# Performance work log

Measured on AMD Instinct MI355X. Metric: run time of the kernel, lower is better.

Reference implementation:

```python
import jax, jax.numpy as jnp
import numpy as np

N_NODES = 30000
N_EDGES = 480000
NODE_DIM = 16
NUM_RADIAL = 8
NUM_ELEMENTS = 120
R_MAX = 5.0
NUM_BLOCKS = 2
N_PATHS = 5  # h0*sh0->0e, h0*sh1->1o, h0*sh2->2e, h1.sh1->0e, h2.sh2->0e


def _sh_basis(u):
    # real spherical harmonics up to l=2, component normalization, on unit vectors u [E,3]
    x, y, z = u[:, 0], u[:, 1], u[:, 2]
    s15 = jnp.sqrt(jnp.asarray(15.0, u.dtype))
    s5 = jnp.sqrt(jnp.asarray(5.0, u.dtype))
    sh1 = jnp.sqrt(jnp.asarray(3.0, u.dtype)) * u                      # [E,3]
    sh2 = jnp.stack([s15 * x * y, s15 * y * z,
                     0.5 * s5 * (3.0 * z * z - 1.0),
                     s15 * x * z, 0.5 * s15 * (x * x - y * y)], -1)    # [E,5]
    return sh1, sh2


def _energy(pos, emb, W_init, Wr, br, W_out, W_read, W1, b1, W2, b2, z, edge_index):
    N = pos.shape[0]
    row, col = edge_index[0], edge_index[1]
    edge_vec = pos[row] - pos[col]                                     # [E,3] gather
    r = jnp.sqrt(jnp.sum(edge_vec * edge_vec, -1) + 1e-12)             # [E]
    n = jnp.arange(1, NUM_RADIAL + 1, dtype=pos.dtype)
    # Bessel radial basis: sqrt(2/rc) * sin(n*pi*r/rc)/r
    radial = jnp.sqrt(2.0 / R_MAX) * jnp.sin(n[None, :] * jnp.pi * r[:, None] / R_MAX) / r[:, None]  # [E,R]
    u = edge_vec / r[:, None]
    sh1, sh2 = _sh_basis(u)

    # initial projection: embedding scalars -> 0e channels; l=1,l=2 start at zero
    h0 = emb[z] @ W_init                                               # [N,C]
    h1 = jnp.zeros((N, NODE_DIM, 3), pos.dtype)
    h2 = jnp.zeros((N, NODE_DIM, 5), pos.dtype)

    for b in range(NUM_BLOCKS):
        w = (radial @ Wr[b] + br[b]).reshape(-1, N_PATHS, NODE_DIM)    # [E,P,C] radial path weights
        h0c, h1c, h2c = h0[col], h1[col], h2[col]
        # scalar messages: h0*sh0 + <h1,sh1> + <h2,sh2>
        m0 = (w[:, 0] * h0c
              + w[:, 3] * jnp.einsum('ecm,em->ec', h1c, sh1)
              + w[:, 4] * jnp.einsum('ecm,em->ec', h2c, sh2))          # [E,C]
        m1 = (w[:, 1] * h0c)[:, :, None] * sh1[:, None, :]             # [E,C,3]
        m2 = (w[:, 2] * h0c)[:, :, None] * sh2[:, None, :]             # [E,C,5]
        a0 = jax.ops.segment_sum(m0, row, num_segments=N)
        a1 = jax.ops.segment_sum(m1, row, num_segments=N)
        a2 = jax.ops.segment_sum(m2, row, num_segments=N)
        h0 = h0 + a0 @ W_out[b, 0]
        h1 = h1 + jnp.einsum('ncm,cd->ndm', a1, W_out[b, 1])
        h2 = h2 + jnp.einsum('ncm,cd->ndm', a2, W_out[b, 2])

    inv = h0 @ W_read                                                  # readout 0e part
    site = jax.nn.silu(inv @ W1 + b1) @ W2 + b2                        # [N,1]
    return jnp.sum(site)


def setup_inputs() -> dict:
    key = jax.random.key(0)
    ks = jax.random.split(key, 12)
    C, R = NODE_DIM, NUM_RADIAL
    s = 1.0 / np.sqrt(C)
    return {
        'pos': jax.random.normal(ks[0], (N_NODES, 3), jnp.float32) * 3.0,
        'z': jax.random.randint(ks[1], (N_NODES,), 0, NUM_ELEMENTS),
        'edge_index': jax.random.randint(ks[2], (2, N_EDGES), 0, N_NODES),
        'emb': jax.random.normal(ks[3], (NUM_ELEMENTS, C), jnp.float32),
        'W_init': jax.random.normal(ks[4], (C, C), jnp.float32) * s,
        'Wr': jax.random.normal(ks[5], (NUM_BLOCKS, R, N_PATHS * C), jnp.float32) / np.sqrt(R),
        'br': jnp.zeros((NUM_BLOCKS, N_PATHS * C), jnp.float32),
        'W_out': jax.random.normal(ks[6], (NUM_BLOCKS, 3, C, C), jnp.float32) * s,
        'W_read': jax.random.normal(ks[7], (C, C), jnp.float32) * s,
        'W1': jax.random.normal(ks[8], (C, C), jnp.float32) * s,
        'b1': jnp.zeros((C,), jnp.float32),
        'W2': jax.random.normal(ks[9], (C, 1), jnp.float32) * s,
        'b2': jnp.zeros((1,), jnp.float32),
    }


def reference(pos, z, edge_index, emb, W_init, Wr, br, W_out, W_read, W1, b1, W2, b2):
    e_fn = lambda p: _energy(p, emb, W_init, Wr, br, W_out, W_read, W1, b1, W2, b2, z, edge_index)
    total, dE_dpos = jax.value_and_grad(e_fn)(pos)
    energy = jnp.reshape(total, (1, 1))
    forces = -dE_dpos
    return energy, forces
```

## Files before the change

### kernel.cpp

```cpp
#include <hip/hip_runtime.h>
#include <math.h>

#ifndef M_PI
#define M_PI 3.14159265358979323846
#endif

static inline int cdiv(int a, int b){ return (a + b - 1) / b; }

#define SQRT3f  1.7320508075688772f
#define SQRT5f  2.23606797749979f
#define SQRT15f 3.872983346207417f
#define KRADf   0.6324555320336759f
#define PI5f    0.6283185307179586f

__device__ __forceinline__ float grp16_sum(float v){
  v += __shfl_xor(v, 1, 64);
  v += __shfl_xor(v, 2, 64);
  v += __shfl_xor(v, 4, 64);
  v += __shfl_xor(v, 8, 64);
  return v;
}
__device__ __forceinline__ float xgrp_sum(float v){
  v += __shfl_xor(v, 16, 64);
  v += __shfl_xor(v, 32, 64);
  return v;
}

__device__ __forceinline__ void sh_from_u(float ux, float uy, float uz,
                                          float* sh1, float* sh2)
{
  sh1[0] = SQRT3f*ux; sh1[1] = SQRT3f*uy; sh1[2] = SQRT3f*uz;
  sh2[0] = SQRT15f*ux*uy;
  sh2[1] = SQRT15f*uy*uz;
  sh2[2] = 0.5f*SQRT5f*(3.f*uz*uz - 1.f);
  sh2[3] = SQRT15f*ux*uz;
  sh2[4] = 0.5f*SQRT15f*(ux*ux - uy*uy);
}

__device__ __forceinline__ void rad_from_sc(float s1, float c1, float inv_r, float* rad)
{
  float tc = 2.f * c1;
  float sprev = 0.f, s = s1;
  float Ki = KRADf * inv_r;
  #pragma unroll
  for (int k = 0; k < 8; k++) {
    rad[k] = Ki * s;
    float sn = tc*s - sprev; sprev = s; s = sn;
  }
}
__device__ __forceinline__ void rad_drad_from_sc(float s1, float c1, float inv_r,
                                                 float* rad, float* draddr)
{
  float tc = 2.f * c1;
  float sprev = 0.f, s = s1, cprev = 1.f, cc = c1;
  float Ki = KRADf * inv_r;
  const float KPI5 = KRADf * PI5f;
  #pragma unroll
  for (int k = 0; k < 8; k++) {
    rad[k] = Ki * s;
    draddr[k] = (KPI5 * (float)(k+1) * cc - rad[k]) * inv_r;
    float sn = tc*s - sprev; sprev = s; s = sn;
    float cn = tc*cc - cprev; cprev = cc; cc = cn;
  }
}

__global__ void k_hist(const int* __restrict__ ei, int E,
                       int* __restrict__ deg_row, int* __restrict__ deg_col)
{
  int e = blockIdx.x * blockDim.x + threadIdx.x;
  if (e >= E) return;
  atomicAdd(&deg_row[ei[e]], 1);
  atomicAdd(&deg_col[ei[E + e]], 1);
}

__global__ void k_alloc(const int* __restrict__ deg_row, const int* __restrict__ deg_col,
                        int* __restrict__ start_row, int* __restrict__ cur_row,
                        int* __restrict__ start_col, int* __restrict__ cur_col,
                        int* __restrict__ cursors, int N)
{
  int idx = blockIdx.x * blockDim.x + threadIdx.x;
  int lane = threadIdx.x & 63;
  #pragma unroll
  for (int which = 0; which < 2; which++) {
    const int* deg = which ? deg_col : deg_row;
    int* start = which ? start_col : start_row;
    int* cur   = which ? cur_col   : cur_row;
    int v = (idx < N) ? deg[idx] : 0;
    int incl = v;
    #pragma unroll
    for (int d = 1; d < 64; d <<= 1) {
      int y = __shfl_up(incl, d, 64);
      if (lane >= d) incl += y;
    }
    int wtot = __shfl(incl, 63, 64);
    int base = 0;
    if (lane == 63) base = atomicAdd(&cursors[which], wtot);
    base = __shfl(base, 63, 64);
    if (idx < N) { int st = base + incl - v; start[idx] = st; cur[idx] = st; }
  }
}

__global__ void k_scatter_geom(const float* __restrict__ pos, const int* __restrict__ ei, int E,
                               int* __restrict__ cur_row, int* __restrict__ cur_col,
                               float4* __restrict__ uR, float2* __restrict__ scR,
                               float4* __restrict__ uC, float2* __restrict__ scC,
                               int* __restrict__ colR, int* __restrict__ cposR,
                               int* __restrict__ rowC, int* __restrict__ rposC)
{
  int e = blockIdx.x * blockDim.x + threadIdx.x;
  if (e >= E) return;
  int row = ei[e], col = ei[E + e];
  int pr = atomicAdd(&cur_row[row], 1);
  int pc = atomicAdd(&cur_col[col], 1);
  colR[pr] = col; cposR[pr] = pc;
  rowC[pc] = row; rposC[pc] = pr;

  float px = pos[row*3+0] - pos[col*3+0];
  float py = pos[row*3+1] - pos[col*3+1];
  float pz = pos[row*3+2] - pos[col*3+2];
  float r2 = px*px + py*py + pz*pz + 1e-12f;
  float r = sqrtf(r2);
  float inv_r = 1.0f / r;
  float ux = px*inv_r, uy = py*inv_r, uz = pz*inv_r;
  float s1, c1;
  sincosf(r * PI5f, &s1, &c1);
  float4 u4 = make_float4(ux, uy, uz, inv_r);
  float2 sc = make_float2(s1, c1);
  uR[pr] = u4; scR[pr] = sc;
  uC[pc] = u4; scC[pc] = sc;
}

__global__ void k_node_init(const float* __restrict__ emb, const int* __restrict__ z,
                            const float* __restrict__ W_init, float* __restrict__ h0, int N)
{
  __shared__ float sW[256];
  if (threadIdx.x < 256) sW[threadIdx.x] = W_init[threadIdx.x];
  __syncthreads();
  int n = blockIdx.x * blockDim.x + threadIdx.x;
  if (n >= N) return;
  const float* e = emb + z[n]*16;
  float ev[16];
  #pragma unroll
  for (int k = 0; k < 16; k++) ev[k] = e[k];
  #pragma unroll
  for (int c = 0; c < 16; c++) {
    float s = 0.f;
    #pragma unroll
    for (int k = 0; k < 16; k++) s += ev[k] * sW[k*16+c];
    h0[n*16+c] = s;
  }
}

__global__ void k_fwd_b0(const float* __restrict__ Wr, const float* __restrict__ br,
                         const float* __restrict__ h0_in,
                         const float4* __restrict__ uR, const float2* __restrict__ scR,
                         const int* __restrict__ colR,
                         const int* __restrict__ start_row, const int* __restrict__ deg_row,
                         float* __restrict__ a0, float* __restrict__ a1, float* __restrict__ a2,
                         int N)
{
  int n = (blockIdx.x * blockDim.x + threadIdx.x) >> 6;
  int lane = threadIdx.x & 63;
  int g = lane >> 4, c = lane & 15;
  if (n >= N) return;
  float wr0[8], wr1[8], wr2[8];
  #pragma unroll
  for (int k = 0; k < 8; k++) {
    wr0[k] = Wr[k*80 + c];
    wr1[k] = Wr[k*80 + 16 + c];
    wr2[k] = Wr[k*80 + 32 + c];
  }
  float b0v = br[c], b1v = br[16 + c], b2v = br[32 + c];

  float acc0 = 0.f, acc1[3] = {0.f,0.f,0.f}, acc2[5] = {0.f,0.f,0.f,0.f,0.f};

  int i0 = start_row[n] + g, i1 = start_row[n] + deg_row[n];
  float4 Un = {0,0,0,0}; float2 SCn = {0,0};
  float h0n = 0.f;
  if (i0 < i1) {
    Un = uR[i0]; SCn = scR[i0];
    h0n = h0_in[colR[i0]*16 + c];
  }
  for (int i = i0; i < i1; i += 4) {
    float4 U = Un; float2 SC = SCn;
    float h0c = h0n;
    if (i+4 < i1) {
      Un = uR[i+4]; SCn = scR[i+4];
      h0n = h0_in[colR[i+4]*16 + c];
    }
    float rad[8];
    rad_from_sc(SC.x, SC.y, U.w, rad);
    float sh1[3], sh2[5];
    sh_from_u(U.x, U.y, U.z, sh1, sh2);
    float w0 = b0v, w1 = b1v, w2 = b2v;
    #pragma unroll
    for (int k = 0; k < 8; k++) {
      w0 += rad[k]*wr0[k]; w1 += rad[k]*wr1[k]; w2 += rad[k]*wr2[k];
    }
    acc0 += w0*h0c;
    float wh1 = w1*h0c, wh2 = w2*h0c;
    #pragma unroll
    for (int m = 0; m < 3; m++) acc1[m] += wh1*sh1[m];
    #pragma unroll
    for (int m = 0; m < 5; m++) acc2[m] += wh2*sh2[m];
  }
  acc0 = xgrp_sum(acc0);
  #pragma unroll
  for (int m = 0; m < 3; m++) acc1[m] = xgrp_sum(acc1[m]);
  #pragma unroll
  for (int m = 0; m < 5; m++) acc2[m] = xgrp_sum(acc2[m]);
  if (g == 0) {
    a0[n*16 + c] = acc0;
    #pragma unroll
    for (int m = 0; m < 3; m++) a1[n*48 + c*3 + m] = acc1[m];
    #pragma unroll
    for (int m = 0; m < 5; m++) a2[n*80 + c*5 + m] = acc2[m];
  }
}

__global__ void k_fwd_b1(const float* __restrict__ Wr, const float* __restrict__ br,
                         const float* __restrict__ h0_in, const float* __restrict__ h1_in,
                         const float* __restrict__ h2_in,
                         const float4* __restrict__ uR, const float2* __restrict__ scR,
                         const int* __restrict__ colR,
                         const int* __restrict__ start_row, const int* __restrict__ deg_row,
                         float* __restrict__ a0, int N)
{
  int n = (blockIdx.x * blockDim.x + threadIdx.x) >> 6;
  int lane = threadIdx.x & 63;
  int g = lane >> 4, c = lane & 15;
  if (n >= N) return;
  float wr0[8], wr3[8], wr4[8];
  #pragma unroll
  for (int k = 0; k < 8; k++) {
    wr0[k] = Wr[k*80 + c];
    wr3[k] = Wr[k*80 + 48 + c];
    wr4[k] = Wr[k*80 + 64 + c];
  }
  float b0v = br[c], b3v = br[48 + c], b4v = br[64 + c];

  float acc0 = 0.f;
  int i0 = start_row[n] + g, i1 = start_row[n] + deg_row[n];
  float4 Un = {0,0,0,0}; float2 SCn = {0,0};
  float h0n = 0.f, h1n[3] = {0,0,0}, h2n[5] = {0,0,0,0,0};
  if (i0 < i1) {
    int col = colR[i0];
    Un = uR[i0]; SCn = scR[i0];
    h0n = h0_in[col*16 + c];
    #pragma unroll
    for (int m = 0; m < 3; m++) h1n[m] = h1_in[col*48 + c*3 + m];
    #pragma unroll
    for (int m = 0; m < 5; m++) h2n[m] = h2_in[col*80 + c*5 + m];
  }
  for (int i = i0; i < i1; i += 4) {
    float4 U = Un; float2 SC = SCn;
    float h0c = h0n;
    float h1c[3], h2c[5];
    #pragma unroll
    for (int m = 0; m < 3; m++) h1c[m] = h1n[m];
    #pragma unroll
    for (int m = 0; m < 5; m++) h2c[m] = h2n[m];
    if (i+4 < i1) {
      int col = colR[i+4];
      Un = uR[i+4]; SCn = scR[i+4];
      h0n = h0_in[col*16 + c];
      #pragma unroll
      for (int m = 0; m < 3; m++) h1n[m] = h1_in[col*48 + c*3 + m];
      #pragma unroll
      for (int m = 0; m < 5; m++) h2n[m] = h2_in[col*80 + c*5 + m];
    }
    float rad[8];
    rad_from_sc(SC.x, SC.y, U.w, rad);
    float sh1[3], sh2[5];
    sh_from_u(U.x, U.y, U.z, sh1, sh2);
    float w0 = b0v, w3 = b3v, w4 = b4v;
    #pragma unroll
    for (int k = 0; k < 8; k++) {
      w0 += rad[k]*wr0[k]; w3 += rad[k]*wr3[k]; w4 += rad[k]*wr4[k];
    }
    float S1 = 0.f, S2 = 0.f;
    #pragma unroll
    for (int m = 0; m < 3; m++) S1 += h1c[m]*sh1[m];
    #pragma unroll
    for (int m = 0; m < 5; m++) S2 += h2c[m]*sh2[m];
    acc0 += w0*h0c + w3*S1 + w4*S2;
  }
  acc0 = xgrp_sum(acc0);
  if (g == 0) a0[n*16 + c] = acc0;
}

__global__ void k_node_update(const float* __restrict__ h0_in,
                              const float* __restrict__ a0, const float* __restrict__ a1,
                              const float* __restrict__ a2,
                              const float* __restrict__ U,
                              float* __restrict__ h0_out, float* __restrict__ h1_out,
                              float* __restrict__ h2_out, int N)
{
  int idx = blockIdx.x * blockDim.x + threadIdx.x;
  int n = idx >> 4, d = idx & 15;
  if (n >= N) return;
  const float* U0 = U;
  const float* U1 = U + 256;
  const float* U2 = U + 512;
  float s = h0_in[n*16 + d];
  #pragma unroll
  for (int c = 0; c < 16; c++) s += a0[n*16 + c] * U0[c*16 + d];
  h0_out[n*16 + d] = s;
  float v1[3] = {0.f, 0.f, 0.f};
  #pragma unroll
  for (int c = 0; c < 16; c++) {
    float u = U1[c*16 + d];
    #pragma unroll
    for (int m = 0; m < 3; m++) v1[m] += a1[n*48 + c*3 + m] * u;
  }
  #pragma unroll
  for (int m = 0; m < 3; m++) h1_out[n*48 + d*3 + m] = v1[m];
  float v2[5] = {0.f, 0.f, 0.f, 0.f, 0.f};
  #pragma unroll
  for (int c = 0; c < 16; c++) {
    float u = U2[c*16 + d];
    #pragma unroll
    for (int m = 0; m < 5; m++) v2[m] += a2[n*80 + c*5 + m] * u;
  }
  #pragma unroll
  for (int m = 0; m < 5; m++) h2_out[n*80 + d*5 + m] = v2[m];
}

__global__ void __launch_bounds__(256, 1)
k_readout_bwd(const float* __restrict__ h0s1, const float* __restrict__ a0in,
              const float* __restrict__ W_read,
              const float* __restrict__ W1, const float* __restrict__ b1,
              const float* __restrict__ W2, const float* __restrict__ b2,
              const float* __restrict__ U0b1,
              float* __restrict__ g0, float* __restrict__ ga0,
              float* __restrict__ partials, int N)
{
  __shared__ float sWr[256], sW1[256], sU[256], sb1[16], sW2[16], sb2;
  __shared__ float swave[4];
  {
    int t = threadIdx.x;
    if (t < 256) { sWr[t] = W_read[t]; sW1[t] = W1[t]; sU[t] = U0b1[t]; }
    if (t < 16)  { sb1[t] = b1[t]; sW2[t] = W2[t]; }
    if (t == 0)  sb2 = b2[0];
  }
  __syncthreads();
  int n = blockIdx.x * blockDim.x + threadIdx.x;
  float site = 0.f;
  if (n < N) {
    float h[16], av[16], inv[16], dt[16], g0v[16];
    #pragma unroll
    for (int d = 0; d < 16; d++) av[d] = a0in[n*16 + d];
    #pragma unroll
    for (int d = 0; d < 16; d++) {
      float s = h0s1[n*16 + d];
      #pragma unroll
      for (int cc = 0; cc < 16; cc++) s += av[cc] * sU[cc*16 + d];
      h[d] = s;
    }
    #pragma unroll
    for (int j = 0; j < 16; j++) {
      float s = 0.f;
      #pragma unroll
      for (int d = 0; d < 16; d++) s += h[d] * sWr[d*16 + j];
      inv[j] = s;
    }
    site = sb2;
    #pragma unroll
    for (int c = 0; c < 16; c++) {
      float t = sb1[c];
      #pragma unroll
      for (int j = 0; j < 16; j++) t += inv[j] * sW1[j*16 + c];
      float sg = 1.f / (1.f + expf(-t));
      float w2v = sW2[c];
      site += t * sg * w2v;
      dt[c] = w2v * sg * (1.f + t * (1.f - sg));
    }
    float dinv[16];
    #pragma unroll
    for (int j = 0; j < 16; j++) {
      float s = 0.f;
      #pragma unroll
      for (int c = 0; c < 16; c++) s += dt[c] * sW1[j*16 + c];
      dinv[j] = s;
    }
    #pragma unroll
    for (int d = 0; d < 16; d++) {
      float s = 0.f;
      #pragma unroll
      for (int j = 0; j < 16; j++) s += dinv[j] * sWr[d*16 + j];
      g0v[d] = s;
      g0[n*16 + d] = s;
    }
    #pragma unroll
    for (int c = 0; c < 16; c++) {
      float s = 0.f;
      #pragma unroll
      for (int d = 0; d < 16; d++) s += g0v[d] * sU[c*16 + d];
      ga0[n*16 + c] = s;
    }
  }
  #pragma unroll
  for (int off = 32; off; off >>= 1) site += __shfl_down(site, off, 64);
  int wave = threadIdx.x >> 6;
  if ((threadIdx.x & 63) == 0) swave[wave] = site;
  __syncthreads();
  if (threadIdx.x == 0)
    partials[blockIdx.x] = swave[0] + swave[1] + swave[2] + swave[3];
}

__global__ void k_energy(const float* __restrict__ partials, int nb,
                         float* __restrict__ energy)
{
  int t = threadIdx.x;
  float s = 0.f;
  for (int i = t; i < nb; i += 128) s += partials[i];
  #pragma unroll
  for (int off = 32; off; off >>= 1) s += __shfl_down(s, off, 64);
  __shared__ float sw[2];
  if ((t & 63) == 0) sw[t >> 6] = s;
  __syncthreads();
  if (t == 0) energy[0] = sw[0] + sw[1];
}

__global__ void k_ga(const float* __restrict__ g0, const float* __restrict__ g1,
                     const float* __restrict__ g2, const float* __restrict__ U,
                     float* __restrict__ ga0, float* __restrict__ ga1, float* __restrict__ ga2,
                     int N)
{
  int idx = blockIdx.x * blockDim.x + threadIdx.x;
  int n = idx >> 4, c = idx & 15;
  if (n >= N) return;
  const float* U0 = U;
  const float* U1 = U + 256;
  const float* U2 = U + 512;
  float s = 0.f;
  #pragma unroll
  for (int d = 0; d < 16; d++) s += g0[n*16 + d] * U0[c*16 + d];
  ga0[n*16 + c] = s;
  float v1[3] = {0.f, 0.f, 0.f};
  #pragma unroll
  for (int d = 0; d < 16; d++) {
    float u = U1[c*16 + d];
    #pragma unroll
    for (int m = 0; m < 3; m++) v1[m] += g1[n*48 + d*3 + m] * u;
  }
  #pragma unroll
  for (int m = 0; m < 3; m++) ga1[n*48 + c*3 + m] = v1[m];
  float v2[5] = {0.f, 0.f, 0.f, 0.f, 0.f};
  #pragma unroll
  for (int d = 0; d < 16; d++) {
    float u = U2[c*16 + d];
    #pragma unroll
    for (int m = 0; m < 5; m++) v2[m] += g2[n*80 + d*5 + m] * u;
  }
  #pragma unroll
  for (int m = 0; m < 5; m++) ga2[n*80 + c*5 + m] = v2[m];
}

__global__ void k_bwd_b1_col(const float* __restrict__ Wr, const float* __restrict__ br,
                             const float* __restrict__ h0_in, const float* __restrict__ h1_in,
                             const float* __restrict__ h2_in,
                             const float* __restrict__ ga0,
                             const float4* __restrict__ uC, const float2* __restrict__ scC,
                             const int* __restrict__ rowC,
                             const int* __restrict__ start_col, const int* __restrict__ deg_col,
                             float* __restrict__ g0, float* __restrict__ g1, float* __restrict__ g2,
                             float* __restrict__ dv_col, int N)
{
  int n = (blockIdx.x * blockDim.x + threadIdx.x) >> 6;
  int lane = threadIdx.x & 63;
  int g = lane >> 4, c = lane & 15;
  if (n >= N) return;
  float wr0[8], wr3[8], wr4[8];
  #pragma unroll
  for (int k = 0; k < 8; k++) {
    wr0[k] = Wr[k*80 + c];
    wr3[k] = Wr[k*80 + 48 + c];
    wr4[k] = Wr[k*80 + 64 + c];
  }
  float b0v = br[c], b3v = br[48 + c], b4v = br[64 + c];

  float h0c = h0_in[n*16 + c];
  float h1c[3], h2c[5];
  #pragma unroll
  for (int m = 0; m < 3; m++) h1c[m] = h1_in[n*48 + c*3 + m];
  #pragma unroll
  for (int m = 0; m < 5; m++) h2c[m] = h2_in[n*80 + c*5 + m];

  float accg0 = 0.f, accg1[3] = {0.f,0.f,0.f}, accg2[5] = {0.f,0.f,0.f,0.f,0.f};

  int i0 = start_col[n] + g, i1 = start_col[n] + deg_col[n];
  float4 Un = {0,0,0,0}; float2 SCn = {0,0};
  float dm0n = 0.f;
  if (i0 < i1) {
    Un = uC[i0]; SCn = scC[i0];
    dm0n = ga0[rowC[i0]*16 + c];
  }
  for (int i = i0; i < i1; i += 4) {
    float4 U = Un; float2 SC = SCn;
    float dm0 = dm0n;
    if (i+4 < i1) {
      Un = uC[i+4]; SCn = scC[i+4];
      dm0n = ga0[rowC[i+4]*16 + c];
    }
    float rad[8], draddr[8];
    rad_drad_from_sc(SC.x, SC.y, U.w, rad, draddr);
    float ux = U.x, uy = U.y, uz = U.z, inv_r = U.w;
    float sh1[3], sh2[5];
    sh_from_u(ux, uy, uz, sh1, sh2);

    float w0 = b0v, w3 = b3v, w4 = b4v;
    #pragma unroll
    for (int k = 0; k < 8; k++) {
      w0 += rad[k]*wr0[k]; w3 += rad[k]*wr3[k]; w4 += rad[k]*wr4[k];
    }

    float S1 = 0.f, S2 = 0.f;
    #pragma unroll
    for (int m = 0; m < 3; m++) S1 += h1c[m]*sh1[m];
    #pragma unroll
    for (int m = 0; m < 5; m++) S2 += h2c[m]*sh2[m];

    float dw0 = dm0 * h0c;
    float dw3 = dm0 * S1;
    float dw4 = dm0 * S2;
    float t3 = dm0 * w3, t4 = dm0 * w4;

    accg0 += dm0 * w0;
    #pragma unroll
    for (int m = 0; m < 3; m++) accg1[m] += t3 * sh1[m];
    #pragma unroll
    for (int m = 0; m < 5; m++) accg2[m] += t4 * sh2[m];

    float q1x = t3*h1c[0], q1y = t3*h1c[1], q1z = t3*h1c[2];
    float q0 = t4*h2c[0], q1 = t4*h2c[1], q2 = t4*h2c[2], q3 = t4*h2c[3], q4 = t4*h2c[4];
    float gr = 0.f;
    #pragma unroll
    for (int k = 0; k < 8; k++)
      gr += (dw0*wr0[k] + dw3*wr3[k] + dw4*wr4[k]) * draddr[k];
    float gux = SQRT3f*q1x + SQRT15f*(uy*q0 + uz*q3 + ux*q4);
    float guy = SQRT3f*q1y + SQRT15f*(ux*q0 + uz*q1 - uy*q4);
    float guz = SQRT3f*q1z + SQRT15f*uy*q1 + 3.f*SQRT5f*uz*q2 + SQRT15f*ux*q3;

    gr  = grp16_sum(gr);
    gux = grp16_sum(gux);
    guy = grp16_sum(guy);
    guz = grp16_sum(guz);

    if (c == 0) {
      float gdotu = gux*ux + guy*uy + guz*uz;
      dv_col[i*3+0] = gr*ux + (gux - gdotu*ux)*inv_r;
      dv_col[i*3+1] = gr*uy + (guy - gdotu*uy)*inv_r;
      dv_col[i*3+2] = gr*uz + (guz - gdotu*uz)*inv_r;
    }
  }
  accg0 = xgrp_sum(accg0);
  #pragma unroll
  for (int m = 0; m < 3; m++) accg1[m] = xgrp_sum(accg1[m]);
  #pragma unroll
  for (int m = 0; m < 5; m++) accg2[m] = xgrp_sum(accg2[m]);
  if (g == 0) {
    g0[n*16 + c] += accg0;
    #pragma unroll
    for (int m = 0; m < 3; m++) g1[n*48 + c*3 + m] = accg1[m];
    #pragma unroll
    for (int m = 0; m < 5; m++) g2[n*80 + c*5 + m] = accg2[m];
  }
}

__global__ void k_bwd_b0_row(const float* __restrict__ Wr, const float* __restrict__ br,
                             const float* __restrict__ h0_in,
                             const float* __restrict__ ga0, const float* __restrict__ ga1,
                             const float* __restrict__ ga2,
                             const float4* __restrict__ uR, const float2* __restrict__ scR,
                             const int* __restrict__ colR,
                             const int* __restrict__ start_row, const int* __restrict__ deg_row,
                             float* __restrict__ dv_row, int N)
{
  int n = (blockIdx.x * blockDim.x + threadIdx.x) >> 6;
  int lane = threadIdx.x & 63;
  int g = lane >> 4, c = lane & 15;
  if (n >= N) return;
  float wr0[8], wr1[8], wr2[8];
  #pragma unroll
  for (int k = 0; k < 8; k++) {
    wr0[k] = Wr[k*80 + c];
    wr1[k] = Wr[k*80 + 16 + c];
    wr2[k] = Wr[k*80 + 32 + c];
  }
  float b1v = br[16 + c], b2v = br[32 + c];

  float dm0 = ga0[n*16 + c];
  float dm1[3], dm2[5];
  #pragma unroll
  for (int m = 0; m < 3; m++) dm1[m] = ga1[n*48 + c*3 + m];
  #pragma unroll
  for (int m = 0; m < 5; m++) dm2[m] = ga2[n*80 + c*5 + m];

  int i0 = start_row[n] + g, i1 = start_row[n] + deg_row[n];
  float4 Un = {0,0,0,0}; float2 SCn = {0,0};
  float h0n = 0.f;
  if (i0 < i1) {
    Un = uR[i0]; SCn = scR[i0];
    h0n = h0_in[colR[i0]*16 + c];
  }
  for (int i = i0; i < i1; i += 4) {
    float4 U = Un; float2 SC = SCn;
    float h0c = h0n;
    if (i+4 < i1) {
      Un = uR[i+4]; SCn = scR[i+4];
      h0n = h0_in[colR[i+4]*16 + c];
    }
    float rad[8], draddr[8];
    rad_drad_from_sc(SC.x, SC.y, U.w, rad, draddr);
    float ux = U.x, uy = U.y, uz = U.z, inv_r = U.w;
    float sh1[3], sh2[5];
    sh_from_u(ux, uy, uz, sh1, sh2);

    float w1 = b1v, w2v = b2v;
    #pragma unroll
    for (int k = 0; k < 8; k++) { w1 += rad[k]*wr1[k]; w2v += rad[k]*wr2[k]; }

    float T1 = 0.f, T2 = 0.f;
    #pragma unroll
    for (int m = 0; m < 3; m++) T1 += dm1[m]*sh1[m];
    #pragma unroll
    for (int m = 0; m < 5; m++) T2 += dm2[m]*sh2[m];

    float dw0 = dm0 * h0c;
    float dw1 = h0c * T1;
    float dw2 = h0c * T2;

    float w1h = w1*h0c, w2h = w2v*h0c;
    float q1x = dm1[0]*w1h, q1y = dm1[1]*w1h, q1z = dm1[2]*w1h;
    float q0 = dm2[0]*w2h, q1 = dm2[1]*w2h, q2 = dm2[2]*w2h, q3 = dm2[3]*w2h, q4 = dm2[4]*w2h;

    float gr = 0.f;
    #pragma unroll
    for (int k = 0; k < 8; k++)
      gr += (dw0*wr0[k] + dw1*wr1[k] + dw2*wr2[k]) * draddr[k];
    float gux = SQRT3f*q1x + SQRT15f*(uy*q0 + uz*q3 + ux*q4);
    float guy = SQRT3f*q1y + SQRT15f*(ux*q0 + uz*q1 - uy*q4);
    float guz = SQRT3f*q1z + SQRT15f*uy*q1 + 3.f*SQRT5f*uz*q2 + SQRT15f*ux*q3;

    gr  = grp16_sum(gr);
    gux = grp16_sum(gux);
    guy = grp16_sum(guy);
    guz = grp16_sum(guz);

    if (c == 0) {
      float gdotu = gux*ux + guy*uy + guz*uz;
      dv_row[i*3+0] = gr*ux + (gux - gdotu*ux)*inv_r;
      dv_row[i*3+1] = gr*uy + (guy - gdotu*uy)*inv_r;
      dv_row[i*3+2] = gr*uz + (guz - gdotu*uz)*inv_r;
    }
  }
}

__global__ void k_force(const int* __restrict__ start_row, const int* __restrict__ deg_row,
                        const int* __restrict__ cposR,
                        const int* __restrict__ start_col, const int* __restrict__ deg_col,
                        const int* __restrict__ rposC,
                        const float* __restrict__ dv_col, const float* __restrict__ dv_row,
                        float* __restrict__ force, int N)
{
  int n = blockIdx.x * blockDim.x + threadIdx.x;
  if (n >= N) return;
  float fx = 0.f, fy = 0.f, fz = 0.f;
  int c0 = start_col[n], c1 = c0 + deg_col[n];
  for (int i = c0; i < c1; i++) {
    int rp = rposC[i];
    fx += dv_col[i*3+0] + dv_row[rp*3+0];
    fy += dv_col[i*3+1] + dv_row[rp*3+1];
    fz += dv_col[i*3+2] + dv_row[rp*3+2];
  }
  int r0 = start_row[n], r1 = r0 + deg_row[n];
  for (int i = r0; i < r1; i++) {
    int cp = cposR[i];
    fx -= dv_row[i*3+0] + dv_col[cp*3+0];
    fy -= dv_row[i*3+1] + dv_col[cp*3+1];
    fz -= dv_row[i*3+2] + dv_col[cp*3+2];
  }
  force[n*3+0] = fx; force[n*3+1] = fy; force[n*3+2] = fz;
}

extern "C" void kernel_launch(void* const* d_in, const int* in_sizes, int n_in,
                              void* d_out, int out_size, void* d_ws, size_t ws_size,
                              hipStream_t stream)
{
  const float* pos    = (const float*)d_in[0];
  const int*   z      = (const int*)  d_in[1];
  const int*   ei     = (const int*)  d_in[2];
  const float* emb    = (const float*)d_in[3];
  const float* W_init = (const float*)d_in[4];
  const float* Wr     = (const float*)d_in[5];
  const float* br     = (const float*)d_in[6];
  const float* W_out  = (const float*)d_in[7];
  const float* W_read = (const float*)d_in[8];
  const float* W1     = (const float*)d_in[9];
  const float* b1     = (const float*)d_in[10];
  const float* W2     = (const float*)d_in[11];
  const float* b2     = (const float*)d_in[12];

  const int N = in_sizes[0] / 3;
  const int E = in_sizes[2] / 2;

  const int BLK = 256;
  const int NPB = BLK / 64;
  const int NB_READOUT = cdiv(N, BLK);

  float* f = (float*)d_ws;
  float4* uR  = (float4*)f; f += (size_t)E*4;
  float4* uC  = (float4*)f; f += (size_t)E*4;
  float2* scR = (float2*)f; f += (size_t)E*2;
  float2* scC = (float2*)f; f += (size_t)E*2;
  float* h0_s0 = f; f += (size_t)N*16;
  float* h0_s1 = f; f += (size_t)N*16;
  float* h1_s1 = f; f += (size_t)N*48;
  float* h2_s1 = f; f += (size_t)N*80;
  float* a0    = f; f += (size_t)N*16;
  float* a1    = f; f += (size_t)N*48;
  float* a2    = f; f += (size_t)N*80;
  float* ga0b1 = f; f += (size_t)N*16;
  float* g0    = f; f += (size_t)N*16;
  float* g1    = f; f += (size_t)N*48;
  float* g2    = f; f += (size_t)N*80;
  float* dv_c  = f; f += (size_t)E*3;
  float* dv_r  = f; f += (size_t)E*3;
  float* partials = f; f += (size_t)NB_READOUT;
  int* ip = (int*)f;
  int* cursors   = ip; ip += 2;
  int* deg_row   = ip; ip += N;
  int* deg_col   = ip; ip += N;
  int* start_row = ip; ip += N;
  int* start_col = ip; ip += N;
  int* cur_row   = ip; ip += N;
  int* cur_col   = ip; ip += N;
  int* colR      = ip; ip += E;
  int* cposR     = ip; ip += E;
  int* rowC      = ip; ip += E;
  int* rposC     = ip; ip += E;

  float* out    = (float*)d_out;
  float* energy = out;
  float* force  = out + 1;

  (void)hipMemsetAsync(cursors, 0, (size_t)(2 + 2*N) * sizeof(int), stream);

  k_hist<<<cdiv(E, BLK), BLK, 0, stream>>>(ei, E, deg_row, deg_col);
  k_alloc<<<cdiv(N, BLK), BLK, 0, stream>>>(deg_row, deg_col, start_row, cur_row,
                                            start_col, cur_col, cursors, N);
  k_scatter_geom<<<cdiv(E, BLK), BLK, 0, stream>>>(pos, ei, E, cur_row, cur_col,
                                                   uR, scR, uC, scC,
                                                   colR, cposR, rowC, rposC);

  k_node_init<<<cdiv(N, BLK), BLK, 0, stream>>>(emb, z, W_init, h0_s0, N);

  k_fwd_b0<<<cdiv(N, NPB), BLK, 0, stream>>>(Wr, br, h0_s0, uR, scR, colR,
                                             start_row, deg_row, a0, a1, a2, N);
  k_node_update<<<cdiv(N*16, BLK), BLK, 0, stream>>>(h0_s0, a0, a1, a2,
                                                     W_out, h0_s1, h1_s1, h2_s1, N);

  k_fwd_b1<<<cdiv(N, NPB), BLK, 0, stream>>>(Wr + 640, br + 80,
                                             h0_s1, h1_s1, h2_s1, uR, scR, colR,
                                             start_row, deg_row, a0, N);

  k_readout_bwd<<<NB_READOUT, BLK, 0, stream>>>(h0_s1, a0, W_read, W1, b1, W2, b2,
                                                W_out + 768, g0, ga0b1, partials, N);
  k_energy<<<1, 128, 0, stream>>>(partials, NB_READOUT, energy);

  k_bwd_b1_col<<<cdiv(N, NPB), BLK, 0, stream>>>(Wr + 640, br + 80,
                                                 h0_s1, h1_s1, h2_s1, ga0b1,
                                                 uC, scC, rowC, start_col, deg_col,
                                                 g0, g1, g2, dv_c, N);

  k_ga<<<cdiv(N*16, BLK), BLK, 0, stream>>>(g0, g1, g2, W_out, a0, a1, a2, N);
  k_bwd_b0_row<<<cdiv(N, NPB), BLK, 0, stream>>>(Wr, br, h0_s0,
                                                 a0, a1, a2, uR, scR, colR,
                                                 start_row, deg_row, dv_r, N);

  k_force<<<cdiv(N, BLK), BLK, 0, stream>>>(start_row, deg_row, cposR,
                                            start_col, deg_col, rposC,
                                            dv_c, dv_r, force, N);
}
```

Before: 497.3 us.

## Use grid-stride persistent waves, 2-channel lanes for edges, and parallel force reduction

Edge kernels become grid-stride loops over nodes with a fixed grid, so the per-lane radial weights are loaded once and reused across many nodes. Three of them map 8 lanes to 2 channels each with float2 loads, letting 8 edges run per wave instead of 4. The backward kernels fold the radial derivative into two scalar accumulators instead of keeping 8-element rad/drad arrays. The force kernel splits each node's edges across 16 lanes and reduces with shuffles. The cost is more registers per lane and a longer per-edge dependency chain.

Result: slower. 899.1 us (+80.8%).

```diff
diff --git a/kernel.cpp b/kernel.cpp
--- a/kernel.cpp
+++ b/kernel.cpp
@@ -12,6 +12,7 @@
 #define SQRT15f 3.872983346207417f
 #define KRADf   0.6324555320336759f
 #define PI5f    0.6283185307179586f
+#define KPI5f   (KRADf * PI5f)
 
 __device__ __forceinline__ float grp16_sum(float v){
   v += __shfl_xor(v, 1, 64);
@@ -20,6 +21,18 @@
   v += __shfl_xor(v, 8, 64);
   return v;
 }
+__device__ __forceinline__ float grp8_sum(float v){
+  v += __shfl_xor(v, 1, 64);
+  v += __shfl_xor(v, 2, 64);
+  v += __shfl_xor(v, 4, 64);
+  return v;
+}
+__device__ __forceinline__ float xgrp8_sum(float v){
+  v += __shfl_xor(v, 8, 64);
+  v += __shfl_xor(v, 16, 64);
+  v += __shfl_xor(v, 32, 64);
+  return v;
+}
 __device__ __forceinline__ float xgrp_sum(float v){
   v += __shfl_xor(v, 16, 64);
   v += __shfl_xor(v, 32, 64);
@@ -48,21 +61,7 @@
     float sn = tc*s - sprev; sprev = s; s = sn;
   }
 }
-__device__ __forceinline__ void rad_drad_from_sc(float s1, float c1, float inv_r,
-                                                 float* rad, float* draddr)
-{
-  float tc = 2.f * c1;
-  float sprev = 0.f, s = s1, cprev = 1.f, cc = c1;
-  float Ki = KRADf * inv_r;
-  const float KPI5 = KRADf * PI5f;
-  #pragma unroll
-  for (int k = 0; k < 8; k++) {
-    rad[k] = Ki * s;
-    draddr[k] = (KPI5 * (float)(k+1) * cc - rad[k]) * inv_r;
-    float sn = tc*s - sprev; sprev = s; s = sn;
-    float cn = tc*cc - cprev; cprev = cc; cc = cn;
-  }
-}
+
 
 __global__ void k_hist(const int* __restrict__ ei, int E,
                        int* __restrict__ deg_row, int* __restrict__ deg_col)
@@ -159,10 +158,10 @@
                          float* __restrict__ a0, float* __restrict__ a1, float* __restrict__ a2,
                          int N)
 {
-  int n = (blockIdx.x * blockDim.x + threadIdx.x) >> 6;
+  int wid = (blockIdx.x * blockDim.x + threadIdx.x) >> 6;
+  int nw  = (gridDim.x * blockDim.x) >> 6;
   int lane = threadIdx.x & 63;
   int g = lane >> 4, c = lane & 15;
-  if (n >= N) return;
   float wr0[8], wr1[8], wr2[8];
   #pragma unroll
   for (int k = 0; k < 8; k++) {
@@ -172,49 +171,51 @@
   }
   float b0v = br[c], b1v = br[16 + c], b2v = br[32 + c];
 
-  float acc0 = 0.f, acc1[3] = {0.f,0.f,0.f}, acc2[5] = {0.f,0.f,0.f,0.f,0.f};
-
-  int i0 = start_row[n] + g, i1 = start_row[n] + deg_row[n];
-  float4 Un = {0,0,0,0}; float2 SCn = {0,0};
-  float h0n = 0.f;
-  if (i0 < i1) {
-    Un = uR[i0]; SCn = scR[i0];
-    h0n = h0_in[colR[i0]*16 + c];
-  }
-  for (int i = i0; i < i1; i += 4) {
-    float4 U = Un; float2 SC = SCn;
-    float h0c = h0n;
-    if (i+4 < i1) {
-      Un = uR[i+4]; SCn = scR[i+4];
-      h0n = h0_in[colR[i+4]*16 + c];
-    }
-    float rad[8];
-    rad_from_sc(SC.x, SC.y, U.w, rad);
-    float sh1[3], sh2[5];
-    sh_from_u(U.x, U.y, U.z, sh1, sh2);
-    float w0 = b0v, w1 = b1v, w2 = b2v;
-    #pragma unroll
-    for (int k = 0; k < 8; k++) {
-      w0 += rad[k]*wr0[k]; w1 += rad[k]*wr1[k]; w2 += rad[k]*wr2[k];
-    }
-    acc0 += w0*h0c;
-    float wh1 = w1*h0c, wh2 = w2*h0c;
-    #pragma unroll
-    for (int m = 0; m < 3; m++) acc1[m] += wh1*sh1[m];
-    #pragma unroll
-    for (int m = 0; m < 5; m++) acc2[m] += wh2*sh2[m];
-  }
-  acc0 = xgrp_sum(acc0);
-  #pragma unroll
-  for (int m = 0; m < 3; m++) acc1[m] = xgrp_sum(acc1[m]);
-  #pragma unroll
-  for (int m = 0; m < 5; m++) acc2[m] = xgrp_sum(acc2[m]);
-  if (g == 0) {
-    a0[n*16 + c] = acc0;
-    #pragma unroll
-    for (int m = 0; m < 3; m++) a1[n*48 + c*3 + m] = acc1[m];
-    #pragma unroll
-    for (int m = 0; m < 5; m++) a2[n*80 + c*5 + m] = acc2[m];
+  for (int n = wid; n < N; n += nw) {
+    float acc0 = 0.f, acc1[3] = {0.f,0.f,0.f}, acc2[5] = {0.f,0.f,0.f,0.f,0.f};
+
+    int i0 = start_row[n] + g, i1 = start_row[n] + deg_row[n];
+    float4 Un = {0,0,0,0}; float2 SCn = {0,0};
+    float h0n = 0.f;
+    if (i0 < i1) {
+      Un = uR[i0]; SCn = scR[i0];
+      h0n = h0_in[colR[i0]*16 + c];
+    }
+    for (int i = i0; i < i1; i += 4) {
+      float4 U = Un; float2 SC = SCn;
+      float h0c = h0n;
+      if (i+4 < i1) {
+        Un = uR[i+4]; SCn = scR[i+4];
+        h0n = h0_in[colR[i+4]*16 + c];
+      }
+      float rad[8];
+      rad_from_sc(SC.x, SC.y, U.w, rad);
+      float sh1[3], sh2[5];
+      sh_from_u(U.x, U.y, U.z, sh1, sh2);
+      float w0 = b0v, w1 = b1v, w2 = b2v;
+      #pragma unroll
+      for (int k = 0; k < 8; k++) {
+        w0 += rad[k]*wr0[k]; w1 += rad[k]*wr1[k]; w2 += rad[k]*wr2[k];
+      }
+      acc0 += w0*h0c;
+      float wh1 = w1*h0c, wh2 = w2*h0c;
+      #pragma unroll
+      for (int m = 0; m < 3; m++) acc1[m] += wh1*sh1[m];
+      #pragma unroll
+      for (int m = 0; m < 5; m++) acc2[m] += wh2*sh2[m];
+    }
+    acc0 = xgrp_sum(acc0);
+    #pragma unroll
+    for (int m = 0; m < 3; m++) acc1[m] = xgrp_sum(acc1[m]);
+    #pragma unroll
+    for (int m = 0; m < 5; m++) acc2[m] = xgrp_sum(acc2[m]);
+    if (g == 0) {
+      a0[n*16 + c] = acc0;
+      #pragma unroll
+      for (int m = 0; m < 3; m++) a1[n*48 + c*3 + m] = acc1[m];
+      #pragma unroll
+      for (int m = 0; m < 5; m++) a2[n*80 + c*5 + m] = acc2[m];
+    }
   }
 }
 
@@ -226,67 +227,77 @@
                          const int* __restrict__ start_row, const int* __restrict__ deg_row,
                          float* __restrict__ a0, int N)
 {
-  int n = (blockIdx.x * blockDim.x + threadIdx.x) >> 6;
+  int wid = (blockIdx.x * blockDim.x + threadIdx.x) >> 6;
+  int nw  = (gridDim.x * blockDim.x) >> 6;
   int lane = threadIdx.x & 63;
-  int g = lane >> 4, c = lane & 15;
-  if (n >= N) return;
-  float wr0[8], wr3[8], wr4[8];
+  int g = lane >> 3, cl = lane & 7;
+  const float2* Wr2 = (const float2*)Wr;
+  const float2* br2 = (const float2*)br;
+  const float2* h0_2 = (const float2*)h0_in;
+  const float2* h1_2 = (const float2*)h1_in;
+  const float2* h2_2 = (const float2*)h2_in;
+
+  float2 wr0[8], wr3[8], wr4[8];
   #pragma unroll
   for (int k = 0; k < 8; k++) {
-    wr0[k] = Wr[k*80 + c];
-    wr3[k] = Wr[k*80 + 48 + c];
-    wr4[k] = Wr[k*80 + 64 + c];
-  }
-  float b0v = br[c], b3v = br[48 + c], b4v = br[64 + c];
-
-  float acc0 = 0.f;
-  int i0 = start_row[n] + g, i1 = start_row[n] + deg_row[n];
-  float4 Un = {0,0,0,0}; float2 SCn = {0,0};
-  float h0n = 0.f, h1n[3] = {0,0,0}, h2n[5] = {0,0,0,0,0};
-  if (i0 < i1) {
-    int col = colR[i0];
-    Un = uR[i0]; SCn = scR[i0];
-    h0n = h0_in[col*16 + c];
-    #pragma unroll
-    for (int m = 0; m < 3; m++) h1n[m] = h1_in[col*48 + c*3 + m];
-    #pragma unroll
-    for (int m = 0; m < 5; m++) h2n[m] = h2_in[col*80 + c*5 + m];
-  }
-  for (int i = i0; i < i1; i += 4) {
-    float4 U = Un; float2 SC = SCn;
-    float h0c = h0n;
-    float h1c[3], h2c[5];
-    #pragma unroll
-    for (int m = 0; m < 3; m++) h1c[m] = h1n[m];
-    #pragma unroll
-    for (int m = 0; m < 5; m++) h2c[m] = h2n[m];
-    if (i+4 < i1) {
-      int col = colR[i+4];
-      Un = uR[i+4]; SCn = scR[i+4];
-      h0n = h0_in[col*16 + c];
-      #pragma unroll
-      for (int m = 0; m < 3; m++) h1n[m] = h1_in[col*48 + c*3 + m];
-      #pragma unroll
-      for (int m = 0; m < 5; m++) h2n[m] = h2_in[col*80 + c*5 + m];
-    }
-    float rad[8];
-    rad_from_sc(SC.x, SC.y, U.w, rad);
-    float sh1[3], sh2[5];
-    sh_from_u(U.x, U.y, U.z, sh1, sh2);
-    float w0 = b0v, w3 = b3v, w4 = b4v;
-    #pragma unroll
-    for (int k = 0; k < 8; k++) {
-      w0 += rad[k]*wr0[k]; w3 += rad[k]*wr3[k]; w4 += rad[k]*wr4[k];
-    }
-    float S1 = 0.f, S2 = 0.f;
-    #pragma unroll
-    for (int m = 0; m < 3; m++) S1 += h1c[m]*sh1[m];
-    #pragma unroll
-    for (int m = 0; m < 5; m++) S2 += h2c[m]*sh2[m];
-    acc0 += w0*h0c + w3*S1 + w4*S2;
-  }
-  acc0 = xgrp_sum(acc0);
-  if (g == 0) a0[n*16 + c] = acc0;
+    wr0[k] = Wr2[k*40 + cl];
+    wr3[k] = Wr2[k*40 + 24 + cl];
+    wr4[k] = Wr2[k*40 + 32 + cl];
+  }
+  float2 b0v = br2[cl], b3v = br2[24 + cl], b4v = br2[32 + cl];
+
+  for (int n = wid; n < N; n += nw) {
+    float acc0x = 0.f, acc0y = 0.f;
+    int i0 = start_row[n] + g, i1 = start_row[n] + deg_row[n];
+    float4 Un = {0,0,0,0}; float2 SCn = {0,0};
+    float2 h0n = {0.f,0.f}; int coln = 0;
+    if (i0 < i1) {
+      coln = colR[i0];
+      Un = uR[i0]; SCn = scR[i0];
+      h0n = h0_2[coln*8 + cl];
+    }
+    for (int i = i0; i < i1; i += 8) {
+      float4 U = Un; float2 SC = SCn; float2 h0c = h0n; int col = coln;
+      if (i+8 < i1) {
+        coln = colR[i+8];
+        Un = uR[i+8]; SCn = scR[i+8];
+        h0n = h0_2[coln*8 + cl];
+      }
+      float2 A0 = h1_2[col*24 + 3*cl + 0];
+      float2 A1 = h1_2[col*24 + 3*cl + 1];
+      float2 A2 = h1_2[col*24 + 3*cl + 2];
+      float2 B0 = h2_2[col*40 + 5*cl + 0];
+      float2 B1 = h2_2[col*40 + 5*cl + 1];
+      float2 B2 = h2_2[col*40 + 5*cl + 2];
+      float2 B3 = h2_2[col*40 + 5*cl + 3];
+      float2 B4 = h2_2[col*40 + 5*cl + 4];
+
+      float inv_r = U.w;
+      float Ki = KRADf * inv_r;
+      float tc = 2.f * SC.y;
+      float sprev = 0.f, s = SC.x;
+      float w0x = b0v.x, w0y = b0v.y, w3x = b3v.x, w3y = b3v.y, w4x = b4v.x, w4y = b4v.y;
+      #pragma unroll
+      for (int k = 0; k < 8; k++) {
+        float rad = Ki * s;
+        w0x += rad*wr0[k].x; w0y += rad*wr0[k].y;
+        w3x += rad*wr3[k].x; w3y += rad*wr3[k].y;
+        w4x += rad*wr4[k].x; w4y += rad*wr4[k].y;
+        float sn = tc*s - sprev; sprev = s; s = sn;
+      }
+      float sh1[3], sh2[5];
+      sh_from_u(U.x, U.y, U.z, sh1, sh2);
+      float S1x = A0.x*sh1[0] + A0.y*sh1[1] + A1.x*sh1[2];
+      float S1y = A1.y*sh1[0] + A2.x*sh1[1] + A2.y*sh1[2];
+      float S2x = B0.x*sh2[0] + B0.y*sh2[1] + B1.x*sh2[2] + B1.y*sh2[3] + B2.x*sh2[4];
+      float S2y = B2.y*sh2[0] + B3.x*sh2[1] + B3.y*sh2[2] + B4.x*sh2[3] + B4.y*sh2[4];
+      acc0x += w0x*h0c.x + w3x*S1x + w4x*S2x;
+      acc0y += w0y*h0c.y + w3y*S1y + w4y*S2y;
+    }
+    acc0x = xgrp8_sum(acc0x);
+    acc0y = xgrp8_sum(acc0y);
+    if (g == 0) ((float2*)a0)[n*8 + cl] = make_float2(acc0x, acc0y);
+  }
 }
 
 __global__ void k_node_update(const float* __restrict__ h0_in,
@@ -467,104 +478,142 @@
                              float* __restrict__ g0, float* __restrict__ g1, float* __restrict__ g2,
                              float* __restrict__ dv_col, int N)
 {
-  int n = (blockIdx.x * blockDim.x + threadIdx.x) >> 6;
+  int wid = (blockIdx.x * blockDim.x + threadIdx.x) >> 6;
+  int nw  = (gridDim.x * blockDim.x) >> 6;
   int lane = threadIdx.x & 63;
-  int g = lane >> 4, c = lane & 15;
-  if (n >= N) return;
-  float wr0[8], wr3[8], wr4[8];
+  int g = lane >> 3, cl = lane & 7;
+  const float2* Wr2 = (const float2*)Wr;
+  const float2* br2 = (const float2*)br;
+  const float2* h0_2 = (const float2*)h0_in;
+  const float2* h1_2 = (const float2*)h1_in;
+  const float2* h2_2 = (const float2*)h2_in;
+  const float2* ga0_2 = (const float2*)ga0;
+
+  float2 wr0[8], wr3[8], wr4[8];
   #pragma unroll
   for (int k = 0; k < 8; k++) {
-    wr0[k] = Wr[k*80 + c];
-    wr3[k] = Wr[k*80 + 48 + c];
-    wr4[k] = Wr[k*80 + 64 + c];
-  }
-  float b0v = br[c], b3v = br[48 + c], b4v = br[64 + c];
-
-  float h0c = h0_in[n*16 + c];
-  float h1c[3], h2c[5];
-  #pragma unroll
-  for (int m = 0; m < 3; m++) h1c[m] = h1_in[n*48 + c*3 + m];
-  #pragma unroll
-  for (int m = 0; m < 5; m++) h2c[m] = h2_in[n*80 + c*5 + m];
-
-  float accg0 = 0.f, accg1[3] = {0.f,0.f,0.f}, accg2[5] = {0.f,0.f,0.f,0.f,0.f};
-
-  int i0 = start_col[n] + g, i1 = start_col[n] + deg_col[n];
-  float4 Un = {0,0,0,0}; float2 SCn = {0,0};
-  float dm0n = 0.f;
-  if (i0 < i1) {
-    Un = uC[i0]; SCn = scC[i0];
-    dm0n = ga0[rowC[i0]*16 + c];
-  }
-  for (int i = i0; i < i1; i += 4) {
-    float4 U = Un; float2 SC = SCn;
-    float dm0 = dm0n;
-    if (i+4 < i1) {
-      Un = uC[i+4]; SCn = scC[i+4];
-      dm0n = ga0[rowC[i+4]*16 + c];
-    }
-    float rad[8], draddr[8];
-    rad_drad_from_sc(SC.x, SC.y, U.w, rad, draddr);
-    float ux = U.x, uy = U.y, uz = U.z, inv_r = U.w;
-    float sh1[3], sh2[5];
-    sh_from_u(ux, uy, uz, sh1, sh2);
-
-    float w0 = b0v, w3 = b3v, w4 = b4v;
-    #pragma unroll
-    for (int k = 0; k < 8; k++) {
-      w0 += rad[k]*wr0[k]; w3 += rad[k]*wr3[k]; w4 += rad[k]*wr4[k];
-    }
-
-    float S1 = 0.f, S2 = 0.f;
-    #pragma unroll
-    for (int m = 0; m < 3; m++) S1 += h1c[m]*sh1[m];
-    #pragma unroll
-    for (int m = 0; m < 5; m++) S2 += h2c[m]*sh2[m];
-
-    float dw0 = dm0 * h0c;
-    float dw3 = dm0 * S1;
-    float dw4 = dm0 * S2;
-    float t3 = dm0 * w3, t4 = dm0 * w4;
-
-    accg0 += dm0 * w0;
-    #pragma unroll
-    for (int m = 0; m < 3; m++) accg1[m] += t3 * sh1[m];
-    #pragma unroll
-    for (int m = 0; m < 5; m++) accg2[m] += t4 * sh2[m];
-
-    float q1x = t3*h1c[0], q1y = t3*h1c[1], q1z = t3*h1c[2];
-    float q0 = t4*h2c[0], q1 = t4*h2c[1], q2 = t4*h2c[2], q3 = t4*h2c[3], q4 = t4*h2c[4];
-    float gr = 0.f;
-    #pragma unroll
-    for (int k = 0; k < 8; k++)
-      gr += (dw0*wr0[k] + dw3*wr3[k] + dw4*wr4[k]) * draddr[k];
-    float gux = SQRT3f*q1x + SQRT15f*(uy*q0 + uz*q3 + ux*q4);
-    float guy = SQRT3f*q1y + SQRT15f*(ux*q0 + uz*q1 - uy*q4);
-    float guz = SQRT3f*q1z + SQRT15f*uy*q1 + 3.f*SQRT5f*uz*q2 + SQRT15f*ux*q3;
-
-    gr  = grp16_sum(gr);
-    gux = grp16_sum(gux);
-    guy = grp16_sum(guy);
-    guz = grp16_sum(guz);
-
-    if (c == 0) {
-      float gdotu = gux*ux + guy*uy + guz*uz;
-      dv_col[i*3+0] = gr*ux + (gux - gdotu*ux)*inv_r;
-      dv_col[i*3+1] = gr*uy + (guy - gdotu*uy)*inv_r;
-      dv_col[i*3+2] = gr*uz + (guz - gdotu*uz)*inv_r;
-    }
-  }
-  accg0 = xgrp_sum(accg0);
-  #pragma unroll
-  for (int m = 0; m < 3; m++) accg1[m] = xgrp_sum(accg1[m]);
-  #pragma unroll
-  for (int m = 0; m < 5; m++) accg2[m] = xgrp_sum(accg2[m]);
-  if (g == 0) {
-    g0[n*16 + c] += accg0;
-    #pragma unroll
-    for (int m = 0; m < 3; m++) g1[n*48 + c*3 + m] = accg1[m];
-    #pragma unroll
-    for (int m = 0; m < 5; m++) g2[n*80 + c*5 + m] = accg2[m];
+    wr0[k] = Wr2[k*40 + cl];
+    wr3[k] = Wr2[k*40 + 24 + cl];
+    wr4[k] = Wr2[k*40 + 32 + cl];
+  }
+  float2 b0v = br2[cl], b3v = br2[24 + cl], b4v = br2[32 + cl];
+
+  for (int n = wid; n < N; n += nw) {
+    float2 h0c = h0_2[n*8 + cl];
+    float2 A0 = h1_2[n*24 + 3*cl + 0];
+    float2 A1 = h1_2[n*24 + 3*cl + 1];
+    float2 A2 = h1_2[n*24 + 3*cl + 2];
+    float h1a[3] = {A0.x, A0.y, A1.x};
+    float h1b[3] = {A1.y, A2.x, A2.y};
+    float2 B0 = h2_2[n*40 + 5*cl + 0];
+    float2 B1 = h2_2[n*40 + 5*cl + 1];
+    float2 B2 = h2_2[n*40 + 5*cl + 2];
+    float2 B3 = h2_2[n*40 + 5*cl + 3];
+    float2 B4 = h2_2[n*40 + 5*cl + 4];
+    float h2a[5] = {B0.x, B0.y, B1.x, B1.y, B2.x};
+    float h2b[5] = {B2.y, B3.x, B3.y, B4.x, B4.y};
+
+    float accg0x = 0.f, accg0y = 0.f;
+    float accg1a[3] = {0.f,0.f,0.f}, accg1b[3] = {0.f,0.f,0.f};
+    float accg2a[5] = {0.f,0.f,0.f,0.f,0.f}, accg2b[5] = {0.f,0.f,0.f,0.f,0.f};
+
+    int i0 = start_col[n] + g, i1 = start_col[n] + deg_col[n];
+    float4 Un = {0,0,0,0}; float2 SCn = {0,0};
+    float2 dm0n = {0.f,0.f};
+    if (i0 < i1) {
+      Un = uC[i0]; SCn = scC[i0];
+      dm0n = ga0_2[rowC[i0]*8 + cl];
+    }
+    for (int i = i0; i < i1; i += 8) {
+      float4 U = Un; float2 SC = SCn; float2 dm0 = dm0n;
+      if (i + 8 < i1) {
+        Un = uC[i+8]; SCn = scC[i+8];
+        dm0n = ga0_2[rowC[i+8]*8 + cl];
+      }
+      float sh1[3], sh2[5];
+      sh_from_u(U.x, U.y, U.z, sh1, sh2);
+      float S1x = h1a[0]*sh1[0] + h1a[1]*sh1[1] + h1a[2]*sh1[2];
+      float S1y = h1b[0]*sh1[0] + h1b[1]*sh1[1] + h1b[2]*sh1[2];
+      float S2x = h2a[0]*sh2[0] + h2a[1]*sh2[1] + h2a[2]*sh2[2] + h2a[3]*sh2[3] + h2a[4]*sh2[4];
+      float S2y = h2b[0]*sh2[0] + h2b[1]*sh2[1] + h2b[2]*sh2[2] + h2b[3]*sh2[3] + h2b[4]*sh2[4];
+      float dw0x = dm0.x*h0c.x, dw0y = dm0.y*h0c.y;
+      float dw3x = dm0.x*S1x,   dw3y = dm0.y*S1y;
+      float dw4x = dm0.x*S2x,   dw4y = dm0.y*S2y;
+
+      float inv_r = U.w;
+      float Ki = KRADf * inv_r;
+      float tc = 2.f * SC.y;
+      float sprev = 0.f, s = SC.x, cprev = 1.f, cc = SC.y;
+      float w0x = b0v.x, w0y = b0v.y, w3x = b3v.x, w3y = b3v.y, w4x = b4v.x, w4y = b4v.y;
+      float P = 0.f, Q = 0.f;
+      #pragma unroll
+      for (int k = 0; k < 8; k++) {
+        float rad = Ki * s;
+        w0x += rad*wr0[k].x; w0y += rad*wr0[k].y;
+        w3x += rad*wr3[k].x; w3y += rad*wr3[k].y;
+        w4x += rad*wr4[k].x; w4y += rad*wr4[k].y;
+        float t = dw0x*wr0[k].x + dw0y*wr0[k].y
+                + dw3x*wr3[k].x + dw3y*wr3[k].y
+                + dw4x*wr4[k].x + dw4y*wr4[k].y;
+        P += (t*cc) * (float)(k+1);
+        Q += t*rad;
+        float sn = tc*s - sprev; sprev = s; s = sn;
+        float cn = tc*cc - cprev; cprev = cc; cc = cn;
+      }
+      accg0x += dm0.x*w0x; accg0y += dm0.y*w0y;
+      float t3x = dm0.x*w3x, t3y = dm0.y*w3y;
+      float t4x = dm0.x*w4x, t4y = dm0.y*w4y;
+      #pragma unroll
+      for (int m = 0; m < 3; m++) { accg1a[m] += t3x*sh1[m]; accg1b[m] += t3y*sh1[m]; }
+      #pragma unroll
+      for (int m = 0; m < 5; m++) { accg2a[m] += t4x*sh2[m]; accg2b[m] += t4y*sh2[m]; }
+
+      float q1x = t3x*h1a[0] + t3y*h1b[0];
+      float q1y = t3x*h1a[1] + t3y*h1b[1];
+      float q1z = t3x*h1a[2] + t3y*h1b[2];
+      float q0 = t4x*h2a[0] + t4y*h2b[0];
+      float q1 = t4x*h2a[1] + t4y*h2b[1];
+      float q2 = t4x*h2a[2] + t4y*h2b[2];
+      float q3 = t4x*h2a[3] + t4y*h2b[3];
+      float q4 = t4x*h2a[4] + t4y*h2b[4];
+
+      float gr = (KPI5f*P - Q) * inv_r;
+      float gux = SQRT3f*q1x + SQRT15f*(U.y*q0 + U.z*q3 + U.x*q4);
+      float guy = SQRT3f*q1y + SQRT15f*(U.x*q0 + U.z*q1 - U.y*q4);
+      float guz = SQRT3f*q1z + SQRT15f*U.y*q1 + 3.f*SQRT5f*U.z*q2 + SQRT15f*U.x*q3;
+
+      gr  = grp8_sum(gr);
+      gux = grp8_sum(gux);
+      guy = grp8_sum(guy);
+      guz = grp8_sum(guz);
+
+      if (cl == 0) {
+        float gdotu = gux*U.x + guy*U.y + guz*U.z;
+        dv_col[i*3+0] = gr*U.x + (gux - gdotu*U.x)*inv_r;
+        dv_col[i*3+1] = gr*U.y + (guy - gdotu*U.y)*inv_r;
+        dv_col[i*3+2] = gr*U.z + (guz - gdotu*U.z)*inv_r;
+      }
+    }
+    accg0x = xgrp8_sum(accg0x); accg0y = xgrp8_sum(accg0y);
+    #pragma unroll
+    for (int m = 0; m < 3; m++) { accg1a[m] = xgrp8_sum(accg1a[m]); accg1b[m] = xgrp8_sum(accg1b[m]); }
+    #pragma unroll
+    for (int m = 0; m < 5; m++) { accg2a[m] = xgrp8_sum(accg2a[m]); accg2b[m] = xgrp8_sum(accg2b[m]); }
+    if (g == 0) {
+      float2* g0_2 = (float2*)g0;
+      float2 old = g0_2[n*8 + cl];
+      g0_2[n*8 + cl] = make_float2(old.x + accg0x, old.y + accg0y);
+      float2* g1_2 = (float2*)g1;
+      g1_2[n*24 + 3*cl + 0] = make_float2(accg1a[0], accg1a[1]);
+      g1_2[n*24 + 3*cl + 1] = make_float2(accg1a[2], accg1b[0]);
+      g1_2[n*24 + 3*cl + 2] = make_float2(accg1b[1], accg1b[2]);
+      float2* g2_2 = (float2*)g2;
+      g2_2[n*40 + 5*cl + 0] = make_float2(accg2a[0], accg2a[1]);
+      g2_2[n*40 + 5*cl + 1] = make_float2(accg2a[2], accg2a[3]);
+      g2_2[n*40 + 5*cl + 2] = make_float2(accg2a[4], accg2b[0]);
+      g2_2[n*40 + 5*cl + 3] = make_float2(accg2b[1], accg2b[2]);
+      g2_2[n*40 + 5*cl + 4] = make_float2(accg2b[3], accg2b[4]);
+    }
   }
 }
 
@@ -577,82 +626,110 @@
                              const int* __restrict__ start_row, const int* __restrict__ deg_row,
                              float* __restrict__ dv_row, int N)
 {
-  int n = (blockIdx.x * blockDim.x + threadIdx.x) >> 6;
+  int wid = (blockIdx.x * blockDim.x + threadIdx.x) >> 6;
+  int nw  = (gridDim.x * blockDim.x) >> 6;
   int lane = threadIdx.x & 63;
-  int g = lane >> 4, c = lane & 15;
-  if (n >= N) return;
-  float wr0[8], wr1[8], wr2[8];
+  int g = lane >> 3, cl = lane & 7;
+  const float2* Wr2 = (const float2*)Wr;
+  const float2* br2 = (const float2*)br;
+  const float2* h0_2 = (const float2*)h0_in;
+  const float2* ga0_2 = (const float2*)ga0;
+  const float2* ga1_2 = (const float2*)ga1;
+  const float2* ga2_2 = (const float2*)ga2;
+
+  float2 wr0[8], wr1[8], wr2[8];
   #pragma unroll
   for (int k = 0; k < 8; k++) {
-    wr0[k] = Wr[k*80 + c];
-    wr1[k] = Wr[k*80 + 16 + c];
-    wr2[k] = Wr[k*80 + 32 + c];
-  }
-  float b1v = br[16 + c], b2v = br[32 + c];
-
-  float dm0 = ga0[n*16 + c];
-  float dm1[3], dm2[5];
-  #pragma unroll
-  for (int m = 0; m < 3; m++) dm1[m] = ga1[n*48 + c*3 + m];
-  #pragma unroll
-  for (int m = 0; m < 5; m++) dm2[m] = ga2[n*80 + c*5 + m];
-
-  int i0 = start_row[n] + g, i1 = start_row[n] + deg_row[n];
-  float4 Un = {0,0,0,0}; float2 SCn = {0,0};
-  float h0n = 0.f;
-  if (i0 < i1) {
-    Un = uR[i0]; SCn = scR[i0];
-    h0n = h0_in[colR[i0]*16 + c];
-  }
-  for (int i = i0; i < i1; i += 4) {
-    float4 U = Un; float2 SC = SCn;
-    float h0c = h0n;
-    if (i+4 < i1) {
-      Un = uR[i+4]; SCn = scR[i+4];
-      h0n = h0_in[colR[i+4]*16 + c];
-    }
-    float rad[8], draddr[8];
-    rad_drad_from_sc(SC.x, SC.y, U.w, rad, draddr);
-    float ux = U.x, uy = U.y, uz = U.z, inv_r = U.w;
-    float sh1[3], sh2[5];
-    sh_from_u(ux, uy, uz, sh1, sh2);
-
-    float w1 = b1v, w2v = b2v;
-    #pragma unroll
-    for (int k = 0; k < 8; k++) { w1 += rad[k]*wr1[k]; w2v += rad[k]*wr2[k]; }
-
-    float T1 = 0.f, T2 = 0.f;
-    #pragma unroll
-    for (int m = 0; m < 3; m++) T1 += dm1[m]*sh1[m];
-    #pragma unroll
-    for (int m = 0; m < 5; m++) T2 += dm2[m]*sh2[m];
-
-    float dw0 = dm0 * h0c;
-    float dw1 = h0c * T1;
-    float dw2 = h0c * T2;
-
-    float w1h = w1*h0c, w2h = w2v*h0c;
-    float q1x = dm1[0]*w1h, q1y = dm1[1]*w1h, q1z = dm1[2]*w1h;
-    float q0 = dm2[0]*w2h, q1 = dm2[1]*w2h, q2 = dm2[2]*w2h, q3 = dm2[3]*w2h, q4 = dm2[4]*w2h;
-
-    float gr = 0.f;
-    #pragma unroll
-    for (int k = 0; k < 8; k++)
-      gr += (dw0*wr0[k] + dw1*wr1[k] + dw2*wr2[k]) * draddr[k];
-    float gux = SQRT3f*q1x + SQRT15f*(uy*q0 + uz*q3 + ux*q4);
-    float guy = SQRT3f*q1y + SQRT15f*(ux*q0 + uz*q1 - uy*q4);
-    float guz = SQRT3f*q1z + SQRT15f*uy*q1 + 3.f*SQRT5f*uz*q2 + SQRT15f*ux*q3;
-
-    gr  = grp16_sum(gr);
-    gux = grp16_sum(gux);
-    guy = grp16_sum(guy);
-    guz = grp16_sum(guz);
-
-    if (c == 0) {
-      float gdotu = gux*ux + guy*uy + guz*uz;
-      dv_row[i*3+0] = gr*ux + (gux - gdotu*ux)*inv_r;
-      dv_row[i*3+1] = gr*uy + (guy - gdotu*uy)*inv_r;
-      dv_row[i*3+2] = gr*uz + (guz - gdotu*uz)*inv_r;
+    wr0[k] = Wr2[k*40 + cl];
+    wr1[k] = Wr2[k*40 + 8 + cl];
+    wr2[k] = Wr2[k*40 + 16 + cl];
+  }
+  float2 b1v = br2[8 + cl], b2v = br2[16 + cl];
+
+  for (int n = wid; n < N; n += nw) {
+    float2 dm0 = ga0_2[n*8 + cl];
+    float2 A0 = ga1_2[n*24 + 3*cl + 0];
+    float2 A1 = ga1_2[n*24 + 3*cl + 1];
+    float2 A2 = ga1_2[n*24 + 3*cl + 2];
+    float dm1a[3] = {A0.x, A0.y, A1.x};
+    float dm1b[3] = {A1.y, A2.x, A2.y};
+    float2 B0 = ga2_2[n*40 + 5*cl + 0];
+    float2 B1 = ga2_2[n*40 + 5*cl + 1];
+    float2 B2 = ga2_2[n*40 + 5*cl + 2];
+    float2 B3 = ga2_2[n*40 + 5*cl + 3];
+    float2 B4 = ga2_2[n*40 + 5*cl + 4];
+    float dm2a[5] = {B0.x, B0.y, B1.x, B1.y, B2.x};
+    float dm2b[5] = {B2.y, B3.x, B3.y, B4.x, B4.y};
+
+    int i0 = start_row[n] + g, i1 = start_row[n] + deg_row[n];
+    float4 Un = {0,0,0,0}; float2 SCn = {0,0};
+    float2 h0n = {0.f,0.f};
+    if (i0 < i1) {
+      Un = uR[i0]; SCn = scR[i0];
+      h0n = h0_2[colR[i0]*8 + cl];
+    }
+    for (int i = i0; i < i1; i += 8) {
+      float4 U = Un; float2 SC = SCn; float2 h0c = h0n;
+      if (i + 8 < i1) {
+        Un = uR[i+8]; SCn = scR[i+8];
+        h0n = h0_2[colR[i+8]*8 + cl];
+      }
+      float sh1[3], sh2[5];
+      sh_from_u(U.x, U.y, U.z, sh1, sh2);
+      float T1x = dm1a[0]*sh1[0] + dm1a[1]*sh1[1] + dm1a[2]*sh1[2];
+      float T1y = dm1b[0]*sh1[0] + dm1b[1]*sh1[1] + dm1b[2]*sh1[2];
+      float T2x = dm2a[0]*sh2[0] + dm2a[1]*sh2[1] + dm2a[2]*sh2[2] + dm2a[3]*sh2[3] + dm2a[4]*sh2[4];
+      float T2y = dm2b[0]*sh2[0] + dm2b[1]*sh2[1] + dm2b[2]*sh2[2] + dm2b[3]*sh2[3] + dm2b[4]*sh2[4];
+      float dw0x = dm0.x*h0c.x, dw0y = dm0.y*h0c.y;
+      float dw1x = h0c.x*T1x,  dw1y = h0c.y*T1y;
+      float dw2x = h0c.x*T2x,  dw2y = h0c.y*T2y;
+
+      float inv_r = U.w;
+      float Ki = KRADf * inv_r;
+      float tc = 2.f * SC.y;
+      float sprev = 0.f, s = SC.x, cprev = 1.f, cc = SC.y;
+      float w1x = b1v.x, w1y = b1v.y, w2x = b2v.x, w2y = b2v.y;
+      float P = 0.f, Q = 0.f;
+      #pragma unroll
+      for (int k = 0; k < 8; k++) {
+        float rad = Ki * s;
+        w1x += rad*wr1[k].x; w1y += rad*wr1[k].y;
+        w2x += rad*wr2[k].x; w2y += rad*wr2[k].y;
+        float t = dw0x*wr0[k].x + dw0y*wr0[k].y
+                + dw1x*wr1[k].x + dw1y*wr1[k].y
+                + dw2x*wr2[k].x + dw2y*wr2[k].y;
+        P += (t*cc) * (float)(k+1);
+        Q += t*rad;
+        float sn = tc*s - sprev; sprev = s; s = sn;
+        float cn = tc*cc - cprev; cprev = cc; cc = cn;
+      }
+      float w1hx = w1x*h0c.x, w1hy = w1y*h0c.y;
+      float w2hx = w2x*h0c.x, w2hy = w2y*h0c.y;
+      float q1x = dm1a[0]*w1hx + dm1b[0]*w1hy;
+      float q1y = dm1a[1]*w1hx + dm1b[1]*w1hy;
+      float q1z = dm1a[2]*w1hx + dm1b[2]*w1hy;
+      float q0 = dm2a[0]*w2hx + dm2b[0]*w2hy;
+      float q1 = dm2a[1]*w2hx + dm2b[1]*w2hy;
+      float q2 = dm2a[2]*w2hx + dm2b[2]*w2hy;
+      float q3 = dm2a[3]*w2hx + dm2b[3]*w2hy;
+      float q4 = dm2a[4]*w2hx + dm2b[4]*w2hy;
+
+      float gr = (KPI5f*P - Q) * inv_r;
+      float gux = SQRT3f*q1x + SQRT15f*(U.y*q0 + U.z*q3 + U.x*q4);
+      float guy = SQRT3f*q1y + SQRT15f*(U.x*q0 + U.z*q1 - U.y*q4);
+      float guz = SQRT3f*q1z + SQRT15f*U.y*q1 + 3.f*SQRT5f*U.z*q2 + SQRT15f*U.x*q3;
+
+      gr  = grp8_sum(gr);
+      gux = grp8_sum(gux);
+      guy = grp8_sum(guy);
+      guz = grp8_sum(guz);
+
+      if (cl == 0) {
+        float gdotu = gux*U.x + guy*U.y + guz*U.z;
+        dv_row[i*3+0] = gr*U.x + (gux - gdotu*U.x)*inv_r;
+        dv_row[i*3+1] = gr*U.y + (guy - gdotu*U.y)*inv_r;
+        dv_row[i*3+2] = gr*U.z + (guz - gdotu*U.z)*inv_r;
+      }
     }
   }
 }
@@ -664,24 +741,28 @@
                         const float* __restrict__ dv_col, const float* __restrict__ dv_row,
                         float* __restrict__ force, int N)
 {
-  int n = blockIdx.x * blockDim.x + threadIdx.x;
+  int idx = blockIdx.x * blockDim.x + threadIdx.x;
+  int n = idx >> 4, l = idx & 15;
   if (n >= N) return;
   float fx = 0.f, fy = 0.f, fz = 0.f;
   int c0 = start_col[n], c1 = c0 + deg_col[n];
-  for (int i = c0; i < c1; i++) {
+  for (int i = c0 + l; i < c1; i += 16) {
     int rp = rposC[i];
     fx += dv_col[i*3+0] + dv_row[rp*3+0];
     fy += dv_col[i*3+1] + dv_row[rp*3+1];
     fz += dv_col[i*3+2] + dv_row[rp*3+2];
   }
   int r0 = start_row[n], r1 = r0 + deg_row[n];
-  for (int i = r0; i < r1; i++) {
+  for (int i = r0 + l; i < r1; i += 16) {
     int cp = cposR[i];
     fx -= dv_row[i*3+0] + dv_col[cp*3+0];
     fy -= dv_row[i*3+1] + dv_col[cp*3+1];
     fz -= dv_row[i*3+2] + dv_col[cp*3+2];
   }
-  force[n*3+0] = fx; force[n*3+1] = fy; force[n*3+2] = fz;
+  fx = grp16_sum(fx); fy = grp16_sum(fy); fz = grp16_sum(fz);
+  if (l == 0) {
+    force[n*3+0] = fx; force[n*3+1] = fy; force[n*3+2] = fz;
+  }
 }
 
 extern "C" void kernel_launch(void* const* d_in, const int* in_sizes, int n_in,
@@ -706,8 +787,8 @@
   const int E = in_sizes[2] / 2;
 
   const int BLK = 256;
-  const int NPB = BLK / 64;
   const int NB_READOUT = cdiv(N, BLK);
+  const int PBLK = (N < 8192*1) ? cdiv(N, 4) : 2048;
 
   float* f = (float*)d_ws;
   float4* uR  = (float4*)f; f += (size_t)E*4;
@@ -756,30 +837,30 @@
 
   k_node_init<<<cdiv(N, BLK), BLK, 0, stream>>>(emb, z, W_init, h0_s0, N);
 
-  k_fwd_b0<<<cdiv(N, NPB), BLK, 0, stream>>>(Wr, br, h0_s0, uR, scR, colR,
-                                             start_row, deg_row, a0, a1, a2, N);
+  k_fwd_b0<<<PBLK, BLK, 0, stream>>>(Wr, br, h0_s0, uR, scR, colR,
+                                     start_row, deg_row, a0, a1, a2, N);
   k_node_update<<<cdiv(N*16, BLK), BLK, 0, stream>>>(h0_s0, a0, a1, a2,
                                                      W_out, h0_s1, h1_s1, h2_s1, N);
 
-  k_fwd_b1<<<cdiv(N, NPB), BLK, 0, stream>>>(Wr + 640, br + 80,
-                                             h0_s1, h1_s1, h2_s1, uR, scR, colR,
-                                             start_row, deg_row, a0, N);
+  k_fwd_b1<<<PBLK, BLK, 0, stream>>>(Wr + 640, br + 80,
+                                     h0_s1, h1_s1, h2_s1, uR, scR, colR,
+                                     start_row, deg_row, a0, N);
 
   k_readout_bwd<<<NB_READOUT, BLK, 0, stream>>>(h0_s1, a0, W_read, W1, b1, W2, b2,
                                                 W_out + 768, g0, ga0b1, partials, N);
   k_energy<<<1, 128, 0, stream>>>(partials, NB_READOUT, energy);
 
-  k_bwd_b1_col<<<cdiv(N, NPB), BLK, 0, stream>>>(Wr + 640, br + 80,
-                                                 h0_s1, h1_s1, h2_s1, ga0b1,
-                                                 uC, scC, rowC, start_col, deg_col,
-                                                 g0, g1, g2, dv_c, N);
+  k_bwd_b1_col<<<PBLK, BLK, 0, stream>>>(Wr + 640, br + 80,
+                                         h0_s1, h1_s1, h2_s1, ga0b1,
+                                         uC, scC, rowC, start_col, deg_col,
+                                         g0, g1, g2, dv_c, N);
 
   k_ga<<<cdiv(N*16, BLK), BLK, 0, stream>>>(g0, g1, g2, W_out, a0, a1, a2, N);
-  k_bwd_b0_row<<<cdiv(N, NPB), BLK, 0, stream>>>(Wr, br, h0_s0,
-                                                 a0, a1, a2, uR, scR, colR,
-                                                 start_row, deg_row, dv_r, N);
-
-  k_force<<<cdiv(N, BLK), BLK, 0, stream>>>(start_row, deg_row, cposR,
-                                            start_col, deg_col, rposC,
-                                            dv_c, dv_r, force, N);
-}
+  k_bwd_b0_row<<<PBLK, BLK, 0, stream>>>(Wr, br, h0_s0,
+                                         a0, a1, a2, uR, scR, colR,
+                                         start_row, deg_row, dv_r, N);
+
+  k_force<<<cdiv(N*16, BLK), BLK, 0, stream>>>(start_row, deg_row, cposR,
+                                               start_col, deg_col, rposC,
+                                               dv_c, dv_r, force, N);
+}
```
